# Kernel optimization log

Measured on AMD Instinct MI355X. Metric: run time of the kernel, lower is better.

## Reference

```python
import jax, jax.numpy as jnp
import numpy as np

B, S, D, H = 2, 2048, 2048, 16
DK = D // H  # 128


def setup_inputs() -> dict:
    key = jax.random.key(0)
    ks = jax.random.split(key, 14)
    scale = 1.0 / np.sqrt(D)
    inp = {
        "query": jax.random.normal(ks[0], (B, S, D), jnp.float32),
        "key": jax.random.normal(ks[1], (B, S, D), jnp.float32),
        "value": jax.random.normal(ks[2], (B, S, D), jnp.float32),
        # Linear params, torch convention: y = x @ W.T + b, W:[out,in]
        "Wq": jax.random.normal(ks[3], (D, D), jnp.float32) * scale,
        "bq": jnp.zeros((D,), jnp.float32),
        "Wk": jax.random.normal(ks[4], (D, D), jnp.float32) * scale,
        "bk": jnp.zeros((D,), jnp.float32),
        "Wv": jax.random.normal(ks[5], (D, D), jnp.float32) * scale,
        "bv": jnp.zeros((D,), jnp.float32),
        "Wo": jax.random.normal(ks[6], (D, D), jnp.float32) * scale,
        "bo": jnp.zeros((D,), jnp.float32),
    }
    return inp


def reference(query, key, value, Wq, bq, Wk, bk, Wv, bv, Wo, bo):
    b, s, d = query.shape
    # QKV projections -> [B, H, S, DK]
    q = (query @ Wq.T + bq).reshape(b, s, H, DK).transpose(0, 2, 1, 3)
    k = (key @ Wk.T + bk).reshape(b, s, H, DK).transpose(0, 2, 1, 3)
    v = (value @ Wv.T + bv).reshape(b, s, H, DK).transpose(0, 2, 1, 3)
    # scaled dot-product scores [B, H, S, S]
    scores = jnp.einsum('bhqd,bhkd->bhqk', q, k) * (1.0 / np.sqrt(DK))
    causal = jnp.tril(jnp.ones((s, s), dtype=bool))  # [S, S], mask==0 above diag
    scores = jnp.where(causal[None, None], scores, jnp.float32(-1e9))
    attn = jax.nn.softmax(scores, axis=-1)  # attn_dropout = identity (eval)
    x = jnp.einsum('bhqk,bhkd->bhqd', attn, v)
    x = x.transpose(0, 2, 1, 3).reshape(b, s, d)
    out = x @ Wo.T + bo  # resid_dropout = identity (eval)
    return (out, attn)
```

## Files before the change

### kernel.cpp

```cpp
#include <hip/hip_runtime.h>


#define BATCH 2
#define S_LEN 2048
#define D_DIM 2048
#define H_NUM 16
#define DKD   128

typedef __attribute__((ext_vector_type(8))) short  short8;
typedef __attribute__((ext_vector_type(4))) short  short4v;
typedef __attribute__((ext_vector_type(4))) float  floatx4;

__device__ __forceinline__ unsigned short f2bf(float f) {
    unsigned int u = __float_as_uint(f);
    u += 0x7fffu + ((u >> 16) & 1u);
    return (unsigned short)(u >> 16);
}

template<typename T>
__device__ __forceinline__ void stage_tile(const T* __restrict__ src, int ld,
                                           int row0, int k0,
                                           unsigned short* __restrict__ dst,
                                           int tid) {
    if constexpr (sizeof(T) == 4) {
        #pragma unroll
        for (int i = 0; i < 4; ++i) {
            int c = tid + i * 256;
            int r = c >> 3, kc = (c & 7) * 4;
            floatx4 v = *(const floatx4*)(src + (size_t)(row0 + r) * ld + k0 + kc);
            short4v p;
            p[0] = (short)f2bf(v[0]); p[1] = (short)f2bf(v[1]);
            p[2] = (short)f2bf(v[2]); p[3] = (short)f2bf(v[3]);
            *(short4v*)(dst + r * 32 + kc) = p;
        }
    } else {
        #pragma unroll
        for (int i = 0; i < 2; ++i) {
            int c = tid + i * 256;
            int r = c >> 2, kc = (c & 3) * 8;
            *(short8*)(dst + r * 32 + kc) =
                *(const short8*)(src + (size_t)(row0 + r) * ld + k0 + kc);
        }
    }
}

enum { M_PROJ_QK = 0, M_PROJ_V = 1, M_SCORES = 2, M_PV = 3, M_OUT = 4 };

template<int MODE, typename TA, typename TB>
__launch_bounds__(256)
__global__ void gemm_abt(const TA* __restrict__ Ag, const TB* __restrict__ Bg,
                         const float* __restrict__ bias, void* __restrict__ Cg,
                         int K, int lda, int ldb, float scale) {
    const int m0 = blockIdx.y * 128;
    const int n0 = blockIdx.x * 128;
    int kEnd = K;
    const TA* Ap = Ag;
    const TB* Bp = Bg;

    if constexpr (MODE == M_SCORES) {
        if (n0 > m0 + 127) return;
        const size_t z = blockIdx.z;
        Ap = Ag + z * (size_t)S_LEN * DKD;
        Bp = Bg + z * (size_t)S_LEN * DKD;
    }
    if constexpr (MODE == M_PV) {
        const size_t z = blockIdx.z;
        Ap = Ag + z * (size_t)S_LEN * S_LEN;
        Bp = Bg + z * (size_t)DKD * S_LEN;
        kEnd = m0 + 128;
    }

    __shared__ __align__(16) unsigned short As[128][32];
    __shared__ __align__(16) unsigned short Bs[128][32];

    const int tid  = threadIdx.x;
    const int lane = tid & 63;
    const int wave = tid >> 6;
    const int quad = lane >> 4;
    const int l16  = lane & 15;
    const int mw   = (wave >> 1) * 64;
    const int nw   = (wave & 1) * 64;

    floatx4 acc[4][4];
    #pragma unroll
    for (int i = 0; i < 4; ++i)
        #pragma unroll
        for (int j = 0; j < 4; ++j)
            acc[i][j] = (floatx4){0.f, 0.f, 0.f, 0.f};

    for (int k0 = 0; k0 < kEnd; k0 += 32) {
        if (k0 > 0) __syncthreads();
        stage_tile<TA>(Ap, lda, m0, k0, &As[0][0], tid);
        stage_tile<TB>(Bp, ldb, n0, k0, &Bs[0][0], tid);
        __syncthreads();

        short8 af[4], bf[4];
        #pragma unroll
        for (int i = 0; i < 4; ++i)
            af[i] = *(const short8*)&As[mw + i * 16 + l16][quad * 8];
        #pragma unroll
        for (int j = 0; j < 4; ++j)
            bf[j] = *(const short8*)&Bs[nw + j * 16 + l16][quad * 8];
        #pragma unroll
        for (int i = 0; i < 4; ++i)
            #pragma unroll
            for (int j = 0; j < 4; ++j)
                acc[i][j] = __builtin_amdgcn_mfma_f32_16x16x32_bf16(
                    af[i], bf[j], acc[i][j], 0, 0, 0);
    }

    #pragma unroll
    for (int i = 0; i < 4; ++i) {
        #pragma unroll
        for (int j = 0; j < 4; ++j) {
            #pragma unroll
            for (int r = 0; r < 4; ++r) {
                const int row = m0 + mw + i * 16 + quad * 4 + r;
                const int col = n0 + nw + j * 16 + l16;
                float v = acc[i][j][r];
                if constexpr (MODE == M_PROJ_QK || MODE == M_PROJ_V) {
                    v += bias[col];
                    const int b = row >> 11, s = row & (S_LEN - 1);
                    const int h = col >> 7,  dk = col & (DKD - 1);
                    unsigned short* o = (unsigned short*)Cg;
                    if constexpr (MODE == M_PROJ_QK)
                        o[((size_t)(b * H_NUM + h) * S_LEN + s) * DKD + dk] = f2bf(v);
                    else
                        o[((size_t)(b * H_NUM + h) * DKD + dk) * S_LEN + s] = f2bf(v);
                } else if constexpr (MODE == M_SCORES) {
                    float* o = (float*)Cg + (size_t)blockIdx.z * S_LEN * S_LEN;
                    o[(size_t)row * S_LEN + col] = v * scale;
                } else if constexpr (MODE == M_PV) {
                    const int z = blockIdx.z, b = z >> 4, h = z & 15;
                    unsigned short* o = (unsigned short*)Cg;
                    o[((size_t)(b * S_LEN + row)) * D_DIM + h * DKD + col] = f2bf(v);
                } else {
                    float* o = (float*)Cg;
                    o[(size_t)row * D_DIM + col] = v + bias[col];
                }
            }
        }
    }
}

__launch_bounds__(256)
__global__ void softmax_causal(float* __restrict__ attn) {
    const int lane = threadIdx.x & 63;
    const int wave = threadIdx.x >> 6;
    const int s = blockIdx.x * 4 + wave;
    float* rowp = attn + ((size_t)blockIdx.y * S_LEN + s) * S_LEN;

    float vals[32];
    float mx = -3.0e38f;
    #pragma unroll
    for (int j = 0; j < 32; ++j) {
        const int idx = lane + j * 64;
        const float v = (idx <= s) ? rowp[idx] : -3.0e38f;
        vals[j] = v;
        mx = fmaxf(mx, v);
    }
    #pragma unroll
    for (int off = 32; off; off >>= 1) mx = fmaxf(mx, __shfl_down(mx, off, 64));
    mx = __shfl(mx, 0, 64);

    float sum = 0.f;
    #pragma unroll
    for (int j = 0; j < 32; ++j) {
        const int idx = lane + j * 64;
        const float e = (idx <= s) ? __expf(vals[j] - mx) : 0.f;
        vals[j] = e;
        sum += e;
    }
    #pragma unroll
    for (int off = 32; off; off >>= 1) sum += __shfl_down(sum, off, 64);
    sum = __shfl(sum, 0, 64);

    const float inv = 1.f / sum;
    #pragma unroll
    for (int j = 0; j < 32; ++j) rowp[lane + j * 64] = vals[j] * inv;
}

extern "C" void kernel_launch(void* const* d_in, const int* in_sizes, int n_in,
                              void* d_out, int out_size, void* d_ws, size_t ws_size,
                              hipStream_t stream) {
    const float* query = (const float*)d_in[0];
    const float* key_  = (const float*)d_in[1];
    const float* value = (const float*)d_in[2];
    const float* Wq = (const float*)d_in[3];
    const float* bq = (const float*)d_in[4];
    const float* Wk = (const float*)d_in[5];
    const float* bk = (const float*)d_in[6];
    const float* Wv = (const float*)d_in[7];
    const float* bv = (const float*)d_in[8];
    const float* Wo = (const float*)d_in[9];
    const float* bo = (const float*)d_in[10];

    float* out  = (float*)d_out;
    float* attn = out + (size_t)BATCH * S_LEN * D_DIM;

    const size_t NE = (size_t)BATCH * S_LEN * D_DIM;
    unsigned short* qb = (unsigned short*)d_ws;
    unsigned short* kb = qb + NE;
    unsigned short* vT = kb + NE;
    unsigned short* xb = vT + NE;

    const dim3 blk(256);
    const float iscale = 0.088388347648318447f;

    const dim3 gproj(D_DIM / 128, (BATCH * S_LEN) / 128, 1);
    gemm_abt<M_PROJ_QK, float, float><<<gproj, blk, 0, stream>>>(
        query, Wq, bq, qb, D_DIM, D_DIM, D_DIM, 1.f);
    gemm_abt<M_PROJ_QK, float, float><<<gproj, blk, 0, stream>>>(
        key_, Wk, bk, kb, D_DIM, D_DIM, D_DIM, 1.f);
    gemm_abt<M_PROJ_V, float, float><<<gproj, blk, 0, stream>>>(
        value, Wv, bv, vT, D_DIM, D_DIM, D_DIM, 1.f);

    const dim3 gsc(S_LEN / 128, S_LEN / 128, BATCH * H_NUM);
    gemm_abt<M_SCORES, unsigned short, unsigned short><<<gsc, blk, 0, stream>>>(
        qb, kb, nullptr, attn, DKD, DKD, DKD, iscale);

    softmax_causal<<<dim3(S_LEN / 4, BATCH * H_NUM), blk, 0, stream>>>(attn);

    const dim3 gpv(1, S_LEN / 128, BATCH * H_NUM);
    gemm_abt<M_PV, float, unsigned short><<<gpv, blk, 0, stream>>>(
        attn, vT, nullptr, xb, S_LEN, S_LEN, S_LEN, 1.f);

    const dim3 gout(D_DIM / 128, (BATCH * S_LEN) / 128, 1);
    gemm_abt<M_OUT, unsigned short, float><<<gout, blk, 0, stream>>>(
        xb, Wo, bo, out, D_DIM, D_DIM, D_DIM, 1.f);
}
```

Before: 1.277 ms.

## Pre-convert fp32 inputs and weights to bf16, stage via direct global-to-LDS loads

Adds a conversion kernel that turns the activations and all four weight matrices into bf16 once per call. The projection and output GEMMs can then stage both operands with global_load_lds 16-byte direct-to-LDS transfers instead of reloading fp32 and converting on every tile. The softmax is also vectorized to float4 loads and stores. This removes repeated fp32 traffic and conversion work from the GEMM inner loops, at the cost of extra conversion passes and workspace.

```diff
diff --git a/kernel.cpp b/kernel.cpp
--- a/kernel.cpp
+++ b/kernel.cpp
@@ -17,30 +17,37 @@
     return (unsigned short)(u >> 16);
 }
 
-template<typename T>
-__device__ __forceinline__ void stage_tile(const T* __restrict__ src, int ld,
-                                           int row0, int k0,
-                                           unsigned short* __restrict__ dst,
-                                           int tid) {
-    if constexpr (sizeof(T) == 4) {
-        #pragma unroll
-        for (int i = 0; i < 4; ++i) {
-            int c = tid + i * 256;
-            int r = c >> 3, kc = (c & 7) * 4;
-            floatx4 v = *(const floatx4*)(src + (size_t)(row0 + r) * ld + k0 + kc);
-            short4v p;
-            p[0] = (short)f2bf(v[0]); p[1] = (short)f2bf(v[1]);
-            p[2] = (short)f2bf(v[2]); p[3] = (short)f2bf(v[3]);
-            *(short4v*)(dst + r * 32 + kc) = p;
-        }
-    } else {
-        #pragma unroll
-        for (int i = 0; i < 2; ++i) {
-            int c = tid + i * 256;
-            int r = c >> 2, kc = (c & 3) * 8;
-            *(short8*)(dst + r * 32 + kc) =
-                *(const short8*)(src + (size_t)(row0 + r) * ld + k0 + kc);
-        }
+__device__ __forceinline__ void gload16(const void* g, void* l) {
+    __builtin_amdgcn_global_load_lds(
+        (const __attribute__((address_space(1))) void*)g,
+        (__attribute__((address_space(3))) void*)l, 16, 0, 0);
+}
+
+__device__ __forceinline__ void stage_lds_bf16(const unsigned short* __restrict__ src,
+                                               int ld, int row0, int k0,
+                                               unsigned short* __restrict__ dst,
+                                               int tid) {
+    #pragma unroll
+    for (int j = 0; j < 2; ++j) {
+        const int c = tid + j * 256;
+        const int r = c >> 2, kc = (c & 3) * 8;
+        gload16(src + (size_t)(row0 + r) * ld + k0 + kc, dst + c * 8);
+    }
+}
+
+__device__ __forceinline__ void stage_cvt_f32(const float* __restrict__ src,
+                                              int ld, int row0, int k0,
+                                              unsigned short* __restrict__ dst,
+                                              int tid) {
+    #pragma unroll
+    for (int i = 0; i < 4; ++i) {
+        int c = tid + i * 256;
+        int r = c >> 3, kc = (c & 7) * 4;
+        floatx4 v = *(const floatx4*)(src + (size_t)(row0 + r) * ld + k0 + kc);
+        short4v p;
+        p[0] = (short)f2bf(v[0]); p[1] = (short)f2bf(v[1]);
+        p[2] = (short)f2bf(v[2]); p[3] = (short)f2bf(v[3]);
+        *(short4v*)(dst + r * 32 + kc) = p;
     }
 }
 
@@ -90,8 +97,14 @@
 
     for (int k0 = 0; k0 < kEnd; k0 += 32) {
         if (k0 > 0) __syncthreads();
-        stage_tile<TA>(Ap, lda, m0, k0, &As[0][0], tid);
-        stage_tile<TB>(Bp, ldb, n0, k0, &Bs[0][0], tid);
+        if constexpr (sizeof(TB) == 2)
+            stage_lds_bf16((const unsigned short*)Bp, ldb, n0, k0, &Bs[0][0], tid);
+        if constexpr (sizeof(TA) == 2)
+            stage_lds_bf16((const unsigned short*)Ap, lda, m0, k0, &As[0][0], tid);
+        if constexpr (sizeof(TA) == 4)
+            stage_cvt_f32((const float*)Ap, lda, m0, k0, &As[0][0], tid);
+        if constexpr (sizeof(TB) == 4)
+            stage_cvt_f32((const float*)Bp, ldb, n0, k0, &Bs[0][0], tid);
         __syncthreads();
 
         short8 af[4], bf[4];
@@ -150,14 +163,19 @@
     const int s = blockIdx.x * 4 + wave;
     float* rowp = attn + ((size_t)blockIdx.y * S_LEN + s) * S_LEN;
 
-    float vals[32];
+    floatx4 vals[8];
     float mx = -3.0e38f;
     #pragma unroll
-    for (int j = 0; j < 32; ++j) {
-        const int idx = lane + j * 64;
-        const float v = (idx <= s) ? rowp[idx] : -3.0e38f;
-        vals[j] = v;
-        mx = fmaxf(mx, v);
+    for (int j = 0; j < 8; ++j) {
+        const int idx = lane * 4 + j * 256;
+        floatx4 t = {-3.0e38f, -3.0e38f, -3.0e38f, -3.0e38f};
+        if (idx <= s) t = *(const floatx4*)(rowp + idx);
+        #pragma unroll
+        for (int e = 0; e < 4; ++e) {
+            const float x = (idx + e <= s) ? t[e] : -3.0e38f;
+            vals[j][e] = x;
+            mx = fmaxf(mx, x);
+        }
     }
     #pragma unroll
     for (int off = 32; off; off >>= 1) mx = fmaxf(mx, __shfl_down(mx, off, 64));
@@ -165,11 +183,14 @@
 
     float sum = 0.f;
     #pragma unroll
-    for (int j = 0; j < 32; ++j) {
-        const int idx = lane + j * 64;
-        const float e = (idx <= s) ? __expf(vals[j] - mx) : 0.f;
-        vals[j] = e;
-        sum += e;
+    for (int j = 0; j < 8; ++j) {
+        const int idx = lane * 4 + j * 256;
+        #pragma unroll
+        for (int e = 0; e < 4; ++e) {
+            const float ev = (idx + e <= s) ? __expf(vals[j][e] - mx) : 0.f;
+            vals[j][e] = ev;
+            sum += ev;
+        }
     }
     #pragma unroll
     for (int off = 32; off; off >>= 1) sum += __shfl_down(sum, off, 64);
@@ -177,7 +198,27 @@
 
     const float inv = 1.f / sum;
     #pragma unroll
-    for (int j = 0; j < 32; ++j) rowp[lane + j * 64] = vals[j] * inv;
+    for (int j = 0; j < 8; ++j) {
+        const int idx = lane * 4 + j * 256;
+        floatx4 o;
+        #pragma unroll
+        for (int e = 0; e < 4; ++e) o[e] = vals[j][e] * inv;
+        *(floatx4*)(rowp + idx) = o;
+    }
+}
+
+__launch_bounds__(256)
+__global__ void cvt_bf16(const float* __restrict__ src,
+                         unsigned short* __restrict__ dst) {
+    const size_t i = ((size_t)blockIdx.x * 256 + threadIdx.x) * 8;
+    const floatx4 a = *(const floatx4*)(src + i);
+    const floatx4 b = *(const floatx4*)(src + i + 4);
+    short8 o;
+    o[0] = (short)f2bf(a[0]); o[1] = (short)f2bf(a[1]);
+    o[2] = (short)f2bf(a[2]); o[3] = (short)f2bf(a[3]);
+    o[4] = (short)f2bf(b[0]); o[5] = (short)f2bf(b[1]);
+    o[6] = (short)f2bf(b[2]); o[7] = (short)f2bf(b[3]);
+    *(short8*)(dst + i) = o;
 }
 
 extern "C" void kernel_launch(void* const* d_in, const int* in_sizes, int n_in,
@@ -199,21 +240,37 @@
     float* attn = out + (size_t)BATCH * S_LEN * D_DIM;
 
     const size_t NE = (size_t)BATCH * S_LEN * D_DIM;
+    const size_t NW = (size_t)D_DIM * D_DIM;
     unsigned short* qb = (unsigned short*)d_ws;
     unsigned short* kb = qb + NE;
     unsigned short* vT = kb + NE;
     unsigned short* xb = vT + NE;
+    unsigned short* qf = xb + NE;
+    unsigned short* kf = qf + NE;
+    unsigned short* vf = kf + NE;
+    unsigned short* wq = vf + NE;
+    unsigned short* wk = wq + NW;
+    unsigned short* wv = wk + NW;
+    unsigned short* wo = wv + NW;
 
     const dim3 blk(256);
     const float iscale = 0.088388347648318447f;
 
+    cvt_bf16<<<dim3(NE / 2048), blk, 0, stream>>>(query, qf);
+    cvt_bf16<<<dim3(NE / 2048), blk, 0, stream>>>(key_,  kf);
+    cvt_bf16<<<dim3(NE / 2048), blk, 0, stream>>>(value, vf);
+    cvt_bf16<<<dim3(NW / 2048), blk, 0, stream>>>(Wq, wq);
+    cvt_bf16<<<dim3(NW / 2048), blk, 0, stream>>>(Wk, wk);
+    cvt_bf16<<<dim3(NW / 2048), blk, 0, stream>>>(Wv, wv);
+    cvt_bf16<<<dim3(NW / 2048), blk, 0, stream>>>(Wo, wo);
+
     const dim3 gproj(D_DIM / 128, (BATCH * S_LEN) / 128, 1);
-    gemm_abt<M_PROJ_QK, float, float><<<gproj, blk, 0, stream>>>(
-        query, Wq, bq, qb, D_DIM, D_DIM, D_DIM, 1.f);
-    gemm_abt<M_PROJ_QK, float, float><<<gproj, blk, 0, stream>>>(
-        key_, Wk, bk, kb, D_DIM, D_DIM, D_DIM, 1.f);
-    gemm_abt<M_PROJ_V, float, float><<<gproj, blk, 0, stream>>>(
-        value, Wv, bv, vT, D_DIM, D_DIM, D_DIM, 1.f);
+    gemm_abt<M_PROJ_QK, unsigned short, unsigned short><<<gproj, blk, 0, stream>>>(
+        qf, wq, bq, qb, D_DIM, D_DIM, D_DIM, 1.f);
+    gemm_abt<M_PROJ_QK, unsigned short, unsigned short><<<gproj, blk, 0, stream>>>(
+        kf, wk, bk, kb, D_DIM, D_DIM, D_DIM, 1.f);
+    gemm_abt<M_PROJ_V, unsigned short, unsigned short><<<gproj, blk, 0, stream>>>(
+        vf, wv, bv, vT, D_DIM, D_DIM, D_DIM, 1.f);
 
     const dim3 gsc(S_LEN / 128, S_LEN / 128, BATCH * H_NUM);
     gemm_abt<M_SCORES, unsigned short, unsigned short><<<gsc, blk, 0, stream>>>(
@@ -226,6 +283,6 @@
         attn, vT, nullptr, xb, S_LEN, S_LEN, S_LEN, 1.f);
 
     const dim3 gout(D_DIM / 128, (BATCH * S_LEN) / 128, 1);
-    gemm_abt<M_OUT, unsigned short, float><<<gout, blk, 0, stream>>>(
-        xb, Wo, bo, out, D_DIM, D_DIM, D_DIM, 1.f);
-}
+    gemm_abt<M_OUT, unsigned short, unsigned short><<<gout, blk, 0, stream>>>(
+        xb, wo, bo, out, D_DIM, D_DIM, D_DIM, 1.f);
+}
```

Result: faster. 1.182 ms (-7.4%).
